# Kernel optimization log

Measured on AMD Instinct MI355X. Metric: run time of the kernel, lower is better.

## Reference

```python
import jax, jax.numpy as jnp
import numpy as np

Q_HEADS, KV_HEADS, DIMS = 16, 4, 1024
HEAD_DIM = DIMS // Q_HEADS          # 64
GROUPS = Q_HEADS // KV_HEADS        # 4
ROPE_BASE = 10000.0


def rope(x):
    # x: (..., s, d) -- standard interleaved rotary embedding, base 10000
    s, d = x.shape[-2], x.shape[-1]
    inv_freq = 1.0 / (ROPE_BASE ** (jnp.arange(0, d, 2, dtype=jnp.float32) / d))
    ang = jnp.arange(s, dtype=jnp.float32)[:, None] * inv_freq[None, :]  # (s, d/2)
    cos, sin = jnp.cos(ang), jnp.sin(ang)
    x1, x2 = x[..., 0::2], x[..., 1::2]
    out = jnp.stack([x1 * cos - x2 * sin, x1 * sin + x2 * cos], axis=-1)
    return out.reshape(x.shape).astype(x.dtype)


def setup_inputs() -> dict:
    key = jax.random.key(0)
    k1, k2, k3, k4, k5, k6 = jax.random.split(key, 6)
    B, S, E = 4, 2048, 1024
    q = jax.random.normal(k1, (B, S, E), dtype=jnp.float32)
    kv = jax.random.normal(k2, (B, S, E), dtype=jnp.float32)
    sc = 1.0 / np.sqrt(E)
    Wq = jax.random.normal(k3, (E, Q_HEADS, HEAD_DIM), dtype=jnp.float32) * sc
    Wk = jax.random.normal(k4, (E, KV_HEADS, HEAD_DIM), dtype=jnp.float32) * sc
    Wv = jax.random.normal(k5, (E, KV_HEADS, HEAD_DIM), dtype=jnp.float32) * sc
    Wo = jax.random.normal(k6, (HEAD_DIM, E), dtype=jnp.float32) / np.sqrt(HEAD_DIM)
    return {"q": q, "kv": kv, "Wq": Wq, "Wk": Wk, "Wv": Wv, "Wo": Wo}


def reference(q, kv, Wq, Wk, Wv, Wo):
    B, S, E = q.shape
    qh = jnp.einsum('bse,ehd->bshd', q, Wq)    # (B,S,Q_HEADS,hd)
    kh = jnp.einsum('bse,ehd->bshd', kv, Wk)   # (B,S,KV_HEADS,hd)
    vh = jnp.einsum('bse,ehd->bshd', kv, Wv)
    # rearrange '... s (h g) d -> ... g h s d' with g=GROUPS (h = KV_HEADS outer)
    qh = qh.reshape(B, S, KV_HEADS, GROUPS, HEAD_DIM).transpose(0, 3, 2, 1, 4)  # (B,g,h,S,d)
    kh = kh.transpose(0, 2, 1, 3)  # (B,h,S,d)
    vh = vh.transpose(0, 2, 1, 3)  # (B,h,S,d)
    qh = rope(qh)
    kh = rope(kh)
    # NOTE: sums over group axis g (faithful to original einsum)
    scores = jnp.einsum('bghsd,bhad->bhsa', qh, kh)
    attn = jax.nn.softmax(scores / (HEAD_DIM ** 0.5), axis=-1)
    out = jnp.einsum('bhsa,bhad->bhsd', attn, vh)  # (B,h,S,d)
    out = out.mean(axis=1)                          # mean over kv heads -> (B,S,d)
    return out @ Wo                                 # (B,S,E)
```

## Files before the change

kernel.cpp:

```cpp
#include <hip/hip_runtime.h>
#include <math.h>

#define SS 2048
#define EE 1024

using bf16x8 = __attribute__((ext_vector_type(8))) short;
using f32x4  = __attribute__((ext_vector_type(4))) float;

__device__ inline short f2bf(float x) {
    unsigned u = __builtin_bit_cast(unsigned, x);
    return (short)((u + 0x7fffu + ((u >> 16) & 1u)) >> 16);
}
__device__ inline short f2bf_r(float x) {
    return (short)((__builtin_bit_cast(unsigned, x) + 0x8000u) >> 16);
}
__device__ inline unsigned pk_bf16(float a, float b) {
    unsigned ua = __builtin_bit_cast(unsigned, a) + 0x8000u;
    unsigned ub = __builtin_bit_cast(unsigned, b) + 0x8000u;
    return __builtin_amdgcn_perm(ub, ua, 0x07060302u);
}

__global__ __launch_bounds__(256) void prep_weights(const float* __restrict__ Wq,
                                                    const float* __restrict__ Wk,
                                                    const float* __restrict__ Wv,
                                                    const float* __restrict__ Wo,
                                                    short* __restrict__ Wall,
                                                    short* __restrict__ Wo4,
                                                    float2* __restrict__ RT) {
    int idx = blockIdx.x * 256 + threadIdx.x;
    int c = idx >> 10, e = idx & 1023;
    int h = c >> 6, d = c & 63;
    const float* p = Wq + (size_t)e * 1024 + h * 256 + d;
    Wall[(size_t)c * 1024 + e] = f2bf(0.18033688011112042f * (p[0] + p[64] + p[128] + p[192]));
    Wall[(size_t)(256 + c) * 1024 + e] = f2bf(Wk[(size_t)e * 256 + c]);
    Wall[(size_t)(512 + c) * 1024 + e] = f2bf(Wv[(size_t)e * 256 + c]);
    Wo4[(size_t)e * 256 + c] = f2bf(0.25f * Wo[(size_t)d * 1024 + e]);
    if (idx < 65536) {
        int s = idx >> 5, ii = idx & 31;
        float freq = __expf(-(float)ii * (9.210340371976184f / 32.0f));
        float sn, cs;
        sincosf((float)s * freq, &sn, &cs);
        RT[idx] = (float2){cs, sn};
    }
}

__global__ __launch_bounds__(256) void proj_kernel(const float* __restrict__ q,
                                                   const float* __restrict__ kv,
                                                   const short* __restrict__ Wall,
                                                   const float2* __restrict__ RT,
                                                   short* __restrict__ Qb,
                                                   short* __restrict__ Kb,
                                                   short* __restrict__ Vt) {
    __shared__ alignas(16) short As[128][72];
    __shared__ alignas(16) short Bs[64][72];
    int tid = threadIdx.x;
    int wave = tid >> 6, lane = tid & 63, quad = lane >> 4, c16 = lane & 15;
    int wm = wave >> 1, wn = wave & 1;
    int m0 = blockIdx.x * 128, n0 = blockIdx.y * 64;
    const float* A = (n0 < 256) ? q : kv;

    f32x4 acc[4][2];
    #pragma unroll
    for (int i = 0; i < 4; i++)
        #pragma unroll
        for (int j = 0; j < 2; j++) acc[i][j] = (f32x4){0.f, 0.f, 0.f, 0.f};

    for (int k0 = 0; k0 < 1024; k0 += 64) {
        #pragma unroll
        for (int i = 0; i < 8; i++) {
            int id = i * 256 + tid, r = id >> 4, ch = id & 15;
            float4 v = *(const float4*)&A[(size_t)(m0 + r) * 1024 + k0 + ch * 4];
            uint2 u;
            u.x = pk_bf16(v.x, v.y);
            u.y = pk_bf16(v.z, v.w);
            *(uint2*)&As[r][ch * 4] = u;
        }
        #pragma unroll
        for (int i = 0; i < 2; i++) {
            int id = i * 256 + tid, r = id >> 3, ch = id & 7;
            *(int4*)&Bs[r][ch * 8] =
                *(const int4*)&Wall[(size_t)(n0 + r) * 1024 + k0 + ch * 8];
        }
        __syncthreads();
        #pragma unroll
        for (int ks = 0; ks < 64; ks += 32) {
            bf16x8 af[4], bfr[2];
            #pragma unroll
            for (int mt = 0; mt < 4; mt++)
                af[mt] = *(const bf16x8*)&As[wm * 64 + mt * 16 + c16][ks + quad * 8];
            #pragma unroll
            for (int nt = 0; nt < 2; nt++)
                bfr[nt] = *(const bf16x8*)&Bs[wn * 32 + nt * 16 + c16][ks + quad * 8];
            #pragma unroll
            for (int mt = 0; mt < 4; mt++)
                #pragma unroll
                for (int nt = 0; nt < 2; nt++)
                    acc[mt][nt] = __builtin_amdgcn_mfma_f32_16x16x32_bf16(
                        af[mt], bfr[nt], acc[mt][nt], 0, 0, 0);
        }
        __syncthreads();
    }
    if (n0 < 512) {
        #pragma unroll
        for (int mt = 0; mt < 4; mt++) {
            #pragma unroll
            for (int nt = 0; nt < 2; nt++) {
                int cl = wn * 32 + nt * 16 + c16;
                int ii = ((n0 + cl) & 63) >> 1;
                float sgn = (lane & 1) ? 1.0f : -1.0f;
                f32x4 v = acc[mt][nt];
                #pragma unroll
                for (int r = 0; r < 4; r++) {
                    int rl = wm * 64 + mt * 16 + quad * 4 + r;
                    float2 cs = RT[((m0 + rl) & (SS - 1)) * 32 + ii];
                    float other = __shfl_xor(v[r], 1);
                    As[rl][cl] = f2bf_r(v[r] * cs.x + sgn * cs.y * other);
                }
            }
        }
        __syncthreads();
        short* dstb = (n0 < 256) ? Qb : Kb;
        int nc0 = n0 & 255;
        #pragma unroll
        for (int i = 0; i < 4; i++) {
            int id = i * 256 + tid, r = id >> 3, ch = id & 7;
            *(int4*)&dstb[(size_t)(m0 + r) * 256 + nc0 + ch * 8] =
                *(const int4*)&As[r][ch * 8];
        }
    } else {
        short (*Lt)[136] = (short(*)[136])&As[0][0];
        #pragma unroll
        for (int mt = 0; mt < 4; mt++) {
            #pragma unroll
            for (int nt = 0; nt < 2; nt++) {
                int cl = wn * 32 + nt * 16 + c16;
                int sl = wm * 64 + mt * 16 + quad * 4;
                f32x4 v = acc[mt][nt];
                uint2 u;
                u.x = pk_bf16(v[0], v[1]);
                u.y = pk_bf16(v[2], v[3]);
                *(uint2*)&Lt[cl][sl] = u;
            }
        }
        __syncthreads();
        int b = m0 >> 11, s0 = m0 & (SS - 1), c0 = n0 - 512;
        #pragma unroll
        for (int i = 0; i < 4; i++) {
            int id = i * 256 + tid, c = id >> 4, ch = id & 15;
            *(int4*)&Vt[((size_t)(b * 256 + c0 + c)) * SS + s0 + ch * 8] =
                *(const int4*)&Lt[c][ch * 8];
        }
    }
}

__global__ __launch_bounds__(256, 5) void attn_kernel(const short* __restrict__ Qb,
                                                      const short* __restrict__ Kb,
                                                      const short* __restrict__ Vt,
                                                      float* __restrict__ Opart,
                                                      float* __restrict__ Lpart) {
    __shared__ alignas(16) short Qs[64][72];
    __shared__ alignas(16) short Ks[64][72], Vs[64][72];
    int tid = threadIdx.x;
    int wave = tid >> 6, lane = tid & 63, quad = lane >> 4, c16 = lane & 15;
    int qt = blockIdx.x, bh = blockIdx.y, kc = blockIdx.z;
    int q0 = qt * 64;
    size_t qkbase = (size_t)(bh >> 2) * SS * 256 + (bh & 3) * 64;
    size_t vtbase = (size_t)(bh * 64) * SS;
    size_t pbase  = (size_t)(kc * 16 + bh) * SS;

    #pragma unroll
    for (int i = 0; i < 2; i++) {
        int id = i * 256 + tid, r = id >> 3, ch = id & 7;
        *(int4*)&Qs[r][ch * 8] = *(const int4*)&Qb[qkbase + (size_t)(q0 + r) * 256 + ch * 8];
    }
    __syncthreads();
    bf16x8 aq0 = *(const bf16x8*)&Qs[wave * 16 + c16][quad * 8];
    bf16x8 aq1 = *(const bf16x8*)&Qs[wave * 16 + c16][32 + quad * 8];
    short (*Ps)[72] = (short (*)[72])Qs[wave * 16];

    float lsum[4] = {0.f, 0.f, 0.f, 0.f};
    f32x4 o[4];
    #pragma unroll
    for (int dt = 0; dt < 4; dt++) o[dt] = (f32x4){0.f, 0.f, 0.f, 0.f};

    for (int kt = 0; kt < 16; kt++) {
        int a0 = kc * 1024 + kt * 64;
        __syncthreads();
        #pragma unroll
        for (int i = 0; i < 2; i++) {
            int id = i * 256 + tid, r = id >> 3, ch = id & 7;
            *(int4*)&Ks[r][ch * 8] =
                *(const int4*)&Kb[qkbase + (size_t)(a0 + r) * 256 + ch * 8];
            *(int4*)&Vs[r][ch * 8] =
                *(const int4*)&Vt[vtbase + (size_t)r * SS + a0 + ch * 8];
        }
        __syncthreads();
        f32x4 sv[4];
        #pragma unroll
        for (int nt = 0; nt < 4; nt++) sv[nt] = (f32x4){0.f, 0.f, 0.f, 0.f};
        #pragma unroll
        for (int nt = 0; nt < 4; nt++) {
            bf16x8 bk0 = *(const bf16x8*)&Ks[nt * 16 + c16][quad * 8];
            bf16x8 bk1 = *(const bf16x8*)&Ks[nt * 16 + c16][32 + quad * 8];
            sv[nt] = __builtin_amdgcn_mfma_f32_16x16x32_bf16(aq0, bk0, sv[nt], 0, 0, 0);
            sv[nt] = __builtin_amdgcn_mfma_f32_16x16x32_bf16(aq1, bk1, sv[nt], 0, 0, 0);
        }
        #pragma unroll
        for (int nt = 0; nt < 4; nt++)
            #pragma unroll
            for (int r = 0; r < 4; r++) sv[nt][r] = __builtin_exp2f(sv[nt][r]);
        #pragma unroll
        for (int r = 0; r < 4; r++)
            lsum[r] += (sv[0][r] + sv[1][r]) + (sv[2][r] + sv[3][r]);
        #pragma unroll
        for (int nt = 0; nt < 4; nt++)
            #pragma unroll
            for (int r = 0; r < 4; r++)
                Ps[quad * 4 + r][nt * 16 + c16] = f2bf_r(sv[nt][r]);
        #pragma unroll
        for (int ks = 0; ks < 64; ks += 32) {
            bf16x8 ap = *(const bf16x8*)&Ps[c16][ks + quad * 8];
            #pragma unroll
            for (int dt = 0; dt < 4; dt++) {
                bf16x8 bv = *(const bf16x8*)&Vs[dt * 16 + c16][ks + quad * 8];
                o[dt] = __builtin_amdgcn_mfma_f32_16x16x32_bf16(ap, bv, o[dt], 0, 0, 0);
            }
        }
    }
    #pragma unroll
    for (int off = 1; off < 16; off <<= 1)
        #pragma unroll
        for (int r = 0; r < 4; r++) lsum[r] += __shfl_xor(lsum[r], off);
    #pragma unroll
    for (int dt = 0; dt < 4; dt++)
        #pragma unroll
        for (int r = 0; r < 4; r++) {
            int row = q0 + wave * 16 + quad * 4 + r;
            Opart[(pbase + row) * 64 + dt * 16 + c16] = o[dt][r];
        }
    if (c16 == 0)
        #pragma unroll
        for (int r = 0; r < 4; r++)
            Lpart[pbase + q0 + wave * 16 + quad * 4 + r] = lsum[r];
}

__global__ __launch_bounds__(256) void outproj_kernel(const float* __restrict__ Op,
                                                      const float* __restrict__ Lp,
                                                      const short* __restrict__ Wo4,
                                                      float* __restrict__ out) {
    __shared__ alignas(16) short As[64][72];
    __shared__ alignas(16) short Bs[128][72];
    int tid = threadIdx.x;
    int wave = tid >> 6, lane = tid & 63, quad = lane >> 4, c16 = lane & 15;
    int wm = wave >> 1, wn = wave & 1;
    int m0 = blockIdx.x * 64, n0 = blockIdx.y * 128;

    f32x4 acc[2][4];
    #pragma unroll
    for (int i = 0; i < 2; i++)
        #pragma unroll
        for (int j = 0; j < 4; j++) acc[i][j] = (f32x4){0.f, 0.f, 0.f, 0.f};

    for (int k0 = 0; k0 < 256; k0 += 64) {
        int h = k0 >> 6;
        #pragma unroll
        for (int i = 0; i < 4; i++) {
            int id = i * 256 + tid, r = id >> 4, ch = id & 15;
            int row = m0 + r, b = row >> 11, s = row & (SS - 1);
            int bh = b * 4 + h;
            size_t pidx = ((size_t)bh * SS + s) * 64 + ch * 4;
            float4 a = *(const float4*)&Op[pidx];
            float4 c = *(const float4*)&Op[pidx + (size_t)16 * SS * 64];
            float l = Lp[(size_t)bh * SS + s] + Lp[(size_t)(16 + bh) * SS + s];
            float rl = __builtin_amdgcn_rcpf(l);
            uint2 u;
            u.x = pk_bf16((a.x + c.x) * rl, (a.y + c.y) * rl);
            u.y = pk_bf16((a.z + c.z) * rl, (a.w + c.w) * rl);
            *(uint2*)&As[r][ch * 4] = u;
        }
        #pragma unroll
        for (int i = 0; i < 4; i++) {
            int id = i * 256 + tid, r = id >> 3, ch = id & 7;
            *(int4*)&Bs[r][ch * 8] =
                *(const int4*)&Wo4[(size_t)(n0 + r) * 256 + k0 + ch * 8];
        }
        __syncthreads();
        #pragma unroll
        for (int ks = 0; ks < 64; ks += 32) {
            bf16x8 af[2], bfr[4];
            #pragma unroll
            for (int mt = 0; mt < 2; mt++)
                af[mt] = *(const bf16x8*)&As[wm * 32 + mt * 16 + c16][ks + quad * 8];
            #pragma unroll
            for (int nt = 0; nt < 4; nt++)
                bfr[nt] = *(const bf16x8*)&Bs[wn * 64 + nt * 16 + c16][ks + quad * 8];
            #pragma unroll
            for (int mt = 0; mt < 2; mt++)
                #pragma unroll
                for (int nt = 0; nt < 4; nt++)
                    acc[mt][nt] = __builtin_amdgcn_mfma_f32_16x16x32_bf16(
                        af[mt], bfr[nt], acc[mt][nt], 0, 0, 0);
        }
        __syncthreads();
    }
    #pragma unroll
    for (int mt = 0; mt < 2; mt++)
        #pragma unroll
        for (int nt = 0; nt < 4; nt++) {
            int col = n0 + wn * 64 + nt * 16 + c16;
            int rowb = m0 + wm * 32 + mt * 16 + quad * 4;
            #pragma unroll
            for (int r = 0; r < 4; r++)
                out[(size_t)(rowb + r) * 1024 + col] = acc[mt][nt][r];
        }
}

extern "C" void kernel_launch(void* const* d_in, const int* in_sizes, int n_in,
                              void* d_out, int out_size, void* d_ws, size_t ws_size,
                              hipStream_t stream) {
    const float* q  = (const float*)d_in[0];
    const float* kv = (const float*)d_in[1];
    const float* Wq = (const float*)d_in[2];
    const float* Wk = (const float*)d_in[3];
    const float* Wv = (const float*)d_in[4];
    const float* Wo = (const float*)d_in[5];
    float* out = (float*)d_out;

    short* Qb    = (short*)d_ws;
    short* Kb    = Qb + 2097152;
    short* Vt    = Kb + 2097152;
    short* Wall  = Vt + 2097152;
    short* Wo4   = Wall + 786432;
    float2* RT   = (float2*)(Wo4 + 262144);
    float* Opart = (float*)(RT + 65536);
    float* Lpart = Opart + 4194304;

    prep_weights<<<1024, 256, 0, stream>>>(Wq, Wk, Wv, Wo, Wall, Wo4, RT);

    proj_kernel<<<dim3(64, 12), 256, 0, stream>>>(q, kv, Wall, RT, Qb, Kb, Vt);

    attn_kernel<<<dim3(32, 16, 2), 256, 0, stream>>>(Qb, Kb, Vt, Opart, Lpart);

    outproj_kernel<<<dim3(128, 8), 256, 0, stream>>>(Opart, Lpart, Wo4, out);
}
```

Baseline: 210.9 us.

## Prefetch next tiles into registers, shrink projection tile, transpose weights via LDS

The weight-prep kernel is rewritten to transpose weights through an LDS tile, so global reads and writes are coalesced instead of strided scalar accesses, and it runs on far fewer blocks. The projection GEMM tile drops from 128 to 64 rows, doubling the grid and adding an occupancy hint. Both the projection and attention kernels now load the next K-step of operands into registers while the current tile is being computed. The prefetch costs extra registers, and the smaller tile gives less reuse of each loaded weight tile.

```diff
diff --git a/kernel.cpp b/kernel.cpp
--- a/kernel.cpp
+++ b/kernel.cpp
@@ -7,10 +7,6 @@
 using bf16x8 = __attribute__((ext_vector_type(8))) short;
 using f32x4  = __attribute__((ext_vector_type(4))) float;
 
-__device__ inline short f2bf(float x) {
-    unsigned u = __builtin_bit_cast(unsigned, x);
-    return (short)((u + 0x7fffu + ((u >> 16) & 1u)) >> 16);
-}
 __device__ inline short f2bf_r(float x) {
     return (short)((__builtin_bit_cast(unsigned, x) + 0x8000u) >> 16);
 }
@@ -20,89 +16,165 @@
     return __builtin_amdgcn_perm(ub, ua, 0x07060302u);
 }
 
-__global__ __launch_bounds__(256) void prep_weights(const float* __restrict__ Wq,
-                                                    const float* __restrict__ Wk,
-                                                    const float* __restrict__ Wv,
-                                                    const float* __restrict__ Wo,
-                                                    short* __restrict__ Wall,
-                                                    short* __restrict__ Wo4,
-                                                    float2* __restrict__ RT) {
-    int idx = blockIdx.x * 256 + threadIdx.x;
-    int c = idx >> 10, e = idx & 1023;
-    int h = c >> 6, d = c & 63;
-    const float* p = Wq + (size_t)e * 1024 + h * 256 + d;
-    Wall[(size_t)c * 1024 + e] = f2bf(0.18033688011112042f * (p[0] + p[64] + p[128] + p[192]));
-    Wall[(size_t)(256 + c) * 1024 + e] = f2bf(Wk[(size_t)e * 256 + c]);
-    Wall[(size_t)(512 + c) * 1024 + e] = f2bf(Wv[(size_t)e * 256 + c]);
-    Wo4[(size_t)e * 256 + c] = f2bf(0.25f * Wo[(size_t)d * 1024 + e]);
-    if (idx < 65536) {
-        int s = idx >> 5, ii = idx & 31;
-        float freq = __expf(-(float)ii * (9.210340371976184f / 32.0f));
-        float sn, cs;
-        sincosf((float)s * freq, &sn, &cs);
-        RT[idx] = (float2){cs, sn};
-    }
-}
-
-__global__ __launch_bounds__(256) void proj_kernel(const float* __restrict__ q,
-                                                   const float* __restrict__ kv,
-                                                   const short* __restrict__ Wall,
-                                                   const float2* __restrict__ RT,
-                                                   short* __restrict__ Qb,
-                                                   short* __restrict__ Kb,
-                                                   short* __restrict__ Vt) {
-    __shared__ alignas(16) short As[128][72];
+__global__ __launch_bounds__(256) void prep_kernel(const float* __restrict__ Wq,
+                                                   const float* __restrict__ Wk,
+                                                   const float* __restrict__ Wv,
+                                                   const float* __restrict__ Wo,
+                                                   short* __restrict__ Wall,
+                                                   short* __restrict__ Wo4,
+                                                   float2* __restrict__ RT) {
+    __shared__ float T[64][65];
+    int bid = blockIdx.x, tid = threadIdx.x;
+    if (bid < 192) {
+        int src = bid >> 6;
+        int j = bid & 63;
+        int et = j & 15, ct = j >> 4;
+        int e0 = et * 64, c0 = ct * 64;
+        #pragma unroll
+        for (int p = 0; p < 4; p++) {
+            int el = p * 16 + (tid >> 4);
+            int c4 = (tid & 15) * 4;
+            float4 v;
+            if (src == 0) {
+                float4 s = {0, 0, 0, 0};
+                #pragma unroll
+                for (int g = 0; g < 4; g++) {
+                    float4 w = *(const float4*)&Wq[(size_t)(e0 + el) * 1024 + ct * 256 + g * 64 + c4];
+                    s.x += w.x; s.y += w.y; s.z += w.z; s.w += w.w;
+                }
+                v.x = s.x * 0.18033688011112042f; v.y = s.y * 0.18033688011112042f;
+                v.z = s.z * 0.18033688011112042f; v.w = s.w * 0.18033688011112042f;
+            } else if (src == 1) {
+                v = *(const float4*)&Wk[(size_t)(e0 + el) * 256 + c0 + c4];
+            } else {
+                v = *(const float4*)&Wv[(size_t)(e0 + el) * 256 + c0 + c4];
+            }
+            T[c4][el] = v.x; T[c4 + 1][el] = v.y; T[c4 + 2][el] = v.z; T[c4 + 3][el] = v.w;
+        }
+        __syncthreads();
+        #pragma unroll
+        for (int p = 0; p < 8; p++) {
+            int c = p * 8 + (tid >> 5);
+            int e2 = (tid & 31) * 2;
+            unsigned u = pk_bf16(T[c][e2], T[c][e2 + 1]);
+            *(unsigned*)&Wall[(size_t)(src * 256 + c0 + c) * 1024 + e0 + e2] = u;
+        }
+    } else if (bid < 208) {
+        int e0 = (bid - 192) * 64;
+        #pragma unroll
+        for (int p = 0; p < 4; p++) {
+            int d = p * 16 + (tid >> 4);
+            int e4 = (tid & 15) * 4;
+            float4 v = *(const float4*)&Wo[(size_t)d * 1024 + e0 + e4];
+            T[e4][d] = v.x; T[e4 + 1][d] = v.y; T[e4 + 2][d] = v.z; T[e4 + 3][d] = v.w;
+        }
+        __syncthreads();
+        #pragma unroll
+        for (int p = 0; p < 8; p++) {
+            int e = p * 8 + (tid >> 5);
+            int d2 = (tid & 31) * 2;
+            unsigned u = pk_bf16(0.25f * T[e][d2], 0.25f * T[e][d2 + 1]);
+            #pragma unroll
+            for (int h = 0; h < 4; h++)
+                *(unsigned*)&Wo4[(size_t)(e0 + e) * 256 + h * 64 + d2] = u;
+        }
+    } else {
+        int gi = (bid - 208) * 256 + tid;
+        #pragma unroll
+        for (int u = 0; u < 8; u++) {
+            int idx = u * 8192 + gi;
+            int s = idx >> 5, ii = idx & 31;
+            float freq = __expf(-(float)ii * (9.210340371976184f / 32.0f));
+            float sn, cs;
+            sincosf((float)s * freq, &sn, &cs);
+            RT[idx] = (float2){cs, sn};
+        }
+    }
+}
+
+__global__ __launch_bounds__(256, 5) void proj_kernel(const float* __restrict__ q,
+                                                      const float* __restrict__ kv,
+                                                      const short* __restrict__ Wall,
+                                                      const float2* __restrict__ RT,
+                                                      short* __restrict__ Qb,
+                                                      short* __restrict__ Kb,
+                                                      short* __restrict__ Vt) {
+    __shared__ alignas(16) short As[64][72];
     __shared__ alignas(16) short Bs[64][72];
     int tid = threadIdx.x;
     int wave = tid >> 6, lane = tid & 63, quad = lane >> 4, c16 = lane & 15;
     int wm = wave >> 1, wn = wave & 1;
-    int m0 = blockIdx.x * 128, n0 = blockIdx.y * 64;
+    int m0 = blockIdx.x * 64, n0 = blockIdx.y * 64;
     const float* A = (n0 < 256) ? q : kv;
 
-    f32x4 acc[4][2];
-    #pragma unroll
-    for (int i = 0; i < 4; i++)
+    f32x4 acc[2][2];
+    #pragma unroll
+    for (int i = 0; i < 2; i++)
         #pragma unroll
         for (int j = 0; j < 2; j++) acc[i][j] = (f32x4){0.f, 0.f, 0.f, 0.f};
 
+    float4 areg[4];
+    int4 breg[2];
+    #pragma unroll
+    for (int i = 0; i < 4; i++) {
+        int id = i * 256 + tid, r = id >> 4, ch = id & 15;
+        areg[i] = *(const float4*)&A[(size_t)(m0 + r) * 1024 + ch * 4];
+    }
+    #pragma unroll
+    for (int i = 0; i < 2; i++) {
+        int id = i * 256 + tid, r = id >> 3, ch = id & 7;
+        breg[i] = *(const int4*)&Wall[(size_t)(n0 + r) * 1024 + ch * 8];
+    }
+
     for (int k0 = 0; k0 < 1024; k0 += 64) {
-        #pragma unroll
-        for (int i = 0; i < 8; i++) {
+        __syncthreads();
+        #pragma unroll
+        for (int i = 0; i < 4; i++) {
             int id = i * 256 + tid, r = id >> 4, ch = id & 15;
-            float4 v = *(const float4*)&A[(size_t)(m0 + r) * 1024 + k0 + ch * 4];
             uint2 u;
-            u.x = pk_bf16(v.x, v.y);
-            u.y = pk_bf16(v.z, v.w);
+            u.x = pk_bf16(areg[i].x, areg[i].y);
+            u.y = pk_bf16(areg[i].z, areg[i].w);
             *(uint2*)&As[r][ch * 4] = u;
         }
         #pragma unroll
         for (int i = 0; i < 2; i++) {
             int id = i * 256 + tid, r = id >> 3, ch = id & 7;
-            *(int4*)&Bs[r][ch * 8] =
-                *(const int4*)&Wall[(size_t)(n0 + r) * 1024 + k0 + ch * 8];
-        }
-        __syncthreads();
+            *(int4*)&Bs[r][ch * 8] = breg[i];
+        }
+        __syncthreads();
+        if (k0 < 960) {
+            #pragma unroll
+            for (int i = 0; i < 4; i++) {
+                int id = i * 256 + tid, r = id >> 4, ch = id & 15;
+                areg[i] = *(const float4*)&A[(size_t)(m0 + r) * 1024 + k0 + 64 + ch * 4];
+            }
+            #pragma unroll
+            for (int i = 0; i < 2; i++) {
+                int id = i * 256 + tid, r = id >> 3, ch = id & 7;
+                breg[i] = *(const int4*)&Wall[(size_t)(n0 + r) * 1024 + k0 + 64 + ch * 8];
+            }
+        }
         #pragma unroll
         for (int ks = 0; ks < 64; ks += 32) {
-            bf16x8 af[4], bfr[2];
-            #pragma unroll
-            for (int mt = 0; mt < 4; mt++)
-                af[mt] = *(const bf16x8*)&As[wm * 64 + mt * 16 + c16][ks + quad * 8];
+            bf16x8 af[2], bfr[2];
+            #pragma unroll
+            for (int mt = 0; mt < 2; mt++)
+                af[mt] = *(const bf16x8*)&As[wm * 32 + mt * 16 + c16][ks + quad * 8];
             #pragma unroll
             for (int nt = 0; nt < 2; nt++)
                 bfr[nt] = *(const bf16x8*)&Bs[wn * 32 + nt * 16 + c16][ks + quad * 8];
             #pragma unroll
-            for (int mt = 0; mt < 4; mt++)
+            for (int mt = 0; mt < 2; mt++)
                 #pragma unroll
                 for (int nt = 0; nt < 2; nt++)
                     acc[mt][nt] = __builtin_amdgcn_mfma_f32_16x16x32_bf16(
                         af[mt], bfr[nt], acc[mt][nt], 0, 0, 0);
         }
-        __syncthreads();
-    }
+    }
+    __syncthreads();
     if (n0 < 512) {
         #pragma unroll
-        for (int mt = 0; mt < 4; mt++) {
+        for (int mt = 0; mt < 2; mt++) {
             #pragma unroll
             for (int nt = 0; nt < 2; nt++) {
                 int cl = wn * 32 + nt * 16 + c16;
@@ -111,7 +183,7 @@
                 f32x4 v = acc[mt][nt];
                 #pragma unroll
                 for (int r = 0; r < 4; r++) {
-                    int rl = wm * 64 + mt * 16 + quad * 4 + r;
+                    int rl = wm * 32 + mt * 16 + quad * 4 + r;
                     float2 cs = RT[((m0 + rl) & (SS - 1)) * 32 + ii];
                     float other = __shfl_xor(v[r], 1);
                     As[rl][cl] = f2bf_r(v[r] * cs.x + sgn * cs.y * other);
@@ -122,33 +194,32 @@
         short* dstb = (n0 < 256) ? Qb : Kb;
         int nc0 = n0 & 255;
         #pragma unroll
-        for (int i = 0; i < 4; i++) {
+        for (int i = 0; i < 2; i++) {
             int id = i * 256 + tid, r = id >> 3, ch = id & 7;
             *(int4*)&dstb[(size_t)(m0 + r) * 256 + nc0 + ch * 8] =
                 *(const int4*)&As[r][ch * 8];
         }
     } else {
-        short (*Lt)[136] = (short(*)[136])&As[0][0];
-        #pragma unroll
-        for (int mt = 0; mt < 4; mt++) {
+        #pragma unroll
+        for (int mt = 0; mt < 2; mt++) {
             #pragma unroll
             for (int nt = 0; nt < 2; nt++) {
                 int cl = wn * 32 + nt * 16 + c16;
-                int sl = wm * 64 + mt * 16 + quad * 4;
+                int sl = wm * 32 + mt * 16 + quad * 4;
                 f32x4 v = acc[mt][nt];
                 uint2 u;
                 u.x = pk_bf16(v[0], v[1]);
                 u.y = pk_bf16(v[2], v[3]);
-                *(uint2*)&Lt[cl][sl] = u;
+                *(uint2*)&As[cl][sl] = u;
             }
         }
         __syncthreads();
         int b = m0 >> 11, s0 = m0 & (SS - 1), c0 = n0 - 512;
         #pragma unroll
-        for (int i = 0; i < 4; i++) {
-            int id = i * 256 + tid, c = id >> 4, ch = id & 15;
+        for (int i = 0; i < 2; i++) {
+            int id = i * 256 + tid, c = id >> 3, ch = id & 7;
             *(int4*)&Vt[((size_t)(b * 256 + c0 + c)) * SS + s0 + ch * 8] =
-                *(const int4*)&Lt[c][ch * 8];
+                *(const int4*)&As[c][ch * 8];
         }
     }
 }
@@ -183,18 +254,35 @@
     #pragma unroll
     for (int dt = 0; dt < 4; dt++) o[dt] = (f32x4){0.f, 0.f, 0.f, 0.f};
 
-    for (int kt = 0; kt < 16; kt++) {
-        int a0 = kc * 1024 + kt * 64;
-        __syncthreads();
+    int4 kreg[2], vreg[2];
+    {
+        int a0 = kc * 1024;
         #pragma unroll
         for (int i = 0; i < 2; i++) {
             int id = i * 256 + tid, r = id >> 3, ch = id & 7;
-            *(int4*)&Ks[r][ch * 8] =
-                *(const int4*)&Kb[qkbase + (size_t)(a0 + r) * 256 + ch * 8];
-            *(int4*)&Vs[r][ch * 8] =
-                *(const int4*)&Vt[vtbase + (size_t)r * SS + a0 + ch * 8];
-        }
-        __syncthreads();
+            kreg[i] = *(const int4*)&Kb[qkbase + (size_t)(a0 + r) * 256 + ch * 8];
+            vreg[i] = *(const int4*)&Vt[vtbase + (size_t)r * SS + a0 + ch * 8];
+        }
+    }
+
+    for (int kt = 0; kt < 16; kt++) {
+        __syncthreads();
+        #pragma unroll
+        for (int i = 0; i < 2; i++) {
+            int id = i * 256 + tid, r = id >> 3, ch = id & 7;
+            *(int4*)&Ks[r][ch * 8] = kreg[i];
+            *(int4*)&Vs[r][ch * 8] = vreg[i];
+        }
+        __syncthreads();
+        if (kt < 15) {
+            int a0 = kc * 1024 + (kt + 1) * 64;
+            #pragma unroll
+            for (int i = 0; i < 2; i++) {
+                int id = i * 256 + tid, r = id >> 3, ch = id & 7;
+                kreg[i] = *(const int4*)&Kb[qkbase + (size_t)(a0 + r) * 256 + ch * 8];
+                vreg[i] = *(const int4*)&Vt[vtbase + (size_t)r * SS + a0 + ch * 8];
+            }
+        }
         f32x4 sv[4];
         #pragma unroll
         for (int nt = 0; nt < 4; nt++) sv[nt] = (f32x4){0.f, 0.f, 0.f, 0.f};
@@ -335,9 +423,9 @@
     float* Opart = (float*)(RT + 65536);
     float* Lpart = Opart + 4194304;
 
-    prep_weights<<<1024, 256, 0, stream>>>(Wq, Wk, Wv, Wo, Wall, Wo4, RT);
-
-    proj_kernel<<<dim3(64, 12), 256, 0, stream>>>(q, kv, Wall, RT, Qb, Kb, Vt);
+    prep_kernel<<<240, 256, 0, stream>>>(Wq, Wk, Wv, Wo, Wall, Wo4, RT);
+
+    proj_kernel<<<dim3(128, 12), 256, 0, stream>>>(q, kv, Wall, RT, Qb, Kb, Vt);
 
     attn_kernel<<<dim3(32, 16, 2), 256, 0, stream>>>(Qb, Kb, Vt, Opart, Lpart);
 
```

New measurement: 291.1 us. 38.0% more time.
